# Kernel optimization log

Hardware: AMD Instinct MI355X
Metric: run time of the kernel (lower is better)

The kernel has to match this reference:

```python
import jax, jax.numpy as jnp
import numpy as np

B, N, DIM = 8, 4096, 768
HEADS = 12
HEAD_DIM = DIM // HEADS  # 64
EXP = 2                  # expansion_ratio
EDIM = EXP * DIM         # 1536


def setup_inputs() -> dict:
    key = jax.random.key(0)
    ks = jax.random.split(key, 7)
    s = lambda fan_in: 1.0 / np.sqrt(fan_in)
    return {
        "x": jax.random.normal(ks[0], (B, N, DIM), jnp.float32),
        "w_q": jax.random.normal(ks[1], (DIM, DIM), jnp.float32) * s(DIM),
        "w_kv": jax.random.normal(ks[2], (DIM, 2 * DIM), jnp.float32) * s(DIM),
        "w_proj": jax.random.normal(ks[3], (EDIM, DIM), jnp.float32) * s(EDIM),
        "b_proj": jax.random.normal(ks[4], (DIM,), jnp.float32) * 0.01,
        "w_lepe": jax.random.normal(ks[5], (EDIM, 1, 3, 3), jnp.float32) * s(9),
        "b_lepe": jax.random.normal(ks[6], (EDIM,), jnp.float32) * 0.01,
    }


def _expand_heads(t):
    # t: (B, M, C). roll last axis by -head_dim//2 (the i=1 step of the
    # head-expansion trick with r_int=2), concat -> (B, M, 2C), then split
    # into 2*HEADS heads of HEAD_DIM and move heads to axis 1.
    rolled = jnp.roll(t, -(HEAD_DIM // 2), axis=-1)
    e = jnp.concatenate([t, rolled], axis=-1)  # (B, M, 2C)
    Bb, M, _ = e.shape
    return jnp.swapaxes(e.reshape(Bb, M, EXP * HEADS, HEAD_DIM), 1, 2)  # (B, 2h, M, d)


def reference(x, w_q, w_kv, w_proj, b_proj, w_lepe, b_lepe):
    Bb, Nn, C = x.shape
    ed = EXP * C
    # kv projection -> k, v: (B, h, N, d)
    kv = (x @ w_kv).reshape(Bb, Nn, 2, HEADS, HEAD_DIM)
    k = jnp.swapaxes(kv[:, :, 0], 1, 2)
    v = jnp.swapaxes(kv[:, :, 1], 1, 2)
    # q projection + head expansion -> (B, 2h, N, d)
    q = x @ w_q
    eq = _expand_heads(q)
    # LePE: depthwise 3x3 conv on expanded_q laid out as (B, 2C, H, W)
    H = int(round(Nn ** 0.5))
    qc = jnp.swapaxes(eq, 2, 3).reshape(Bb, ed, H, H)
    lepe = jax.lax.conv_general_dilated(
        qc, w_lepe, window_strides=(1, 1), padding='SAME',
        dimension_numbers=('NCHW', 'OIHW', 'NCHW'), feature_group_count=ed)
    lepe = (lepe + b_lepe[None, :, None, None]).reshape(Bb, ed, Nn)
    lepe = jnp.swapaxes(lepe, 1, 2)  # (B, N, 2C)
    # linear attention: softmax over head_dim, precompute K^T V (d x d)
    ks = jax.nn.softmax(k, axis=3)                      # softmax over feature dim d
    ktv = jnp.einsum('bhnd,bhne->bhde', ks, v)          # (B, h, d, d)
    ektv = _expand_heads(jnp.swapaxes(ktv, 1, 2).reshape(Bb, HEAD_DIM, C))  # (B, 2h, d, d)
    attn = jnp.einsum('bhnd,bhde->bhne', eq, ektv)      # (B, 2h, N, d)
    scale = HEAD_DIM ** -0.5
    out = jnp.swapaxes(scale * attn, 1, 2).reshape(Bb, Nn, ed)  # (B, N, 2C)
    return (out + lepe) @ w_proj + b_proj
```

## Files before the change

kernel.cpp:

```cpp
#include <hip/hip_runtime.h>

#define NB 8
#define NTOK 4096
#define CDIM 768
#define EDIM 1536
#define NHEADS 12
#define HD 64
#define TOTTOK (NB * NTOK)
#define KSPLIT 8

typedef float floatx4 __attribute__((ext_vector_type(4)));
typedef __bf16 bf16x8 __attribute__((ext_vector_type(8)));

__device__ __forceinline__ void gld16(const __bf16* g, void* l) {
  __builtin_amdgcn_global_load_lds(
      (const __attribute__((address_space(1))) unsigned int*)g,
      (__attribute__((address_space(3))) unsigned int*)l, 16, 0, 0);
}

#define MFMA16(a, b, c) __builtin_amdgcn_mfma_f32_16x16x32_bf16(a, b, c, 0, 0, 0)
#define FENCE() asm volatile("" ::: "memory")
#define BARRIER() do { FENCE(); __builtin_amdgcn_s_barrier(); FENCE(); } while (0)

__global__ __launch_bounds__(256) void f32_to_bf16_kernel(
    const float* __restrict__ in, __bf16* __restrict__ out, long n) {
  long i = ((long)blockIdx.x * 256 + threadIdx.x) * 4;
  if (i >= n) return;
  float4 f = *(const float4*)(in + i);
  alignas(8) __bf16 h[4];
  h[0] = (__bf16)f.x; h[1] = (__bf16)f.y; h[2] = (__bf16)f.z; h[3] = (__bf16)f.w;
  *(unsigned long long*)(out + i) = *(const unsigned long long*)h;
}

__global__ __launch_bounds__(256) void transpose_w_kernel(
    const float* __restrict__ W, __bf16* __restrict__ Wt, int K, int N) {
  __shared__ float tile[32][33];
  int nb = blockIdx.x * 32, kb = blockIdx.y * 32;
  int tx = threadIdx.x & 31, ty = threadIdx.x >> 5;
  #pragma unroll
  for (int i = ty; i < 32; i += 8)
    tile[i][tx] = W[(long)(kb + i) * N + nb + tx];
  __syncthreads();
  #pragma unroll
  for (int i = ty; i < 32; i += 8)
    Wt[(long)(nb + i) * K + kb + tx] = (__bf16)tile[tx][i];
}

__global__ __launch_bounds__(512, 2) void gemm256_kernel(
    const __bf16* __restrict__ A, const __bf16* __restrict__ Bt,
    void* __restrict__ C0, void* __restrict__ C1,
    const float* __restrict__ bias,
    int M, int N, int K, int nxb, int mode) {
  __shared__ __bf16 As[2][256 * 64];
  __shared__ __bf16 Bs[2][256 * 64];
  const int tid = threadIdx.x;
  const int wave = tid >> 6, lane = tid & 63;

  const int flat = blockIdx.x;
  const int xcd = flat & 7, rem = flat >> 3;
  const int per = (M >> 8) >> 3;
  const int yb = xcd * per + rem / nxb;
  const int xb = rem % nxb;
  const long m0 = (long)yb * 256;
  const int n0 = xb * 256;

  const int wm = (wave >> 2) * 128;
  const int wn = (wave & 3) * 64;

  const int srow = lane >> 3;
  const int gchunk = (lane & 7) ^ srow;
  const __bf16* Ag = A + (m0 + wave * 8 + srow) * (long)K + gchunk * 8;
  const __bf16* Bg = Bt + ((long)n0 + wave * 8 + srow) * (long)K + gchunk * 8;
  const long slabK = 64 * (long)K;

  const int fr = lane & 15, qh = lane >> 4;
  const int c0 = ((qh ^ (fr & 7)) << 3);
  const int c1 = (((qh + 4) ^ (fr & 7)) << 3);

  floatx4 acc[8][4] = {};
  bf16x8 afl[4][2], bf01[2][2], bf23[2][2];
  const int nt = K >> 6;

  {
    char* al = (char*)&As[0][0] + wave * 1024;
    char* bl = (char*)&Bs[0][0] + wave * 1024;
    gld16(Bg + 0 * slabK, bl + 0 * 8192);
    gld16(Bg + 1 * slabK, bl + 1 * 8192);
    gld16(Bg + 2 * slabK, bl + 2 * 8192);
    gld16(Bg + 3 * slabK, bl + 3 * 8192);
    gld16(Ag + 0 * slabK, al + 0 * 8192);
    gld16(Ag + 2 * slabK, al + 2 * 8192);
    gld16(Ag + 1 * slabK, al + 1 * 8192);
    gld16(Ag + 3 * slabK, al + 3 * 8192);
  }
  asm volatile("s_waitcnt vmcnt(2)" ::: "memory");
  BARRIER();

  for (int t = 0; t < nt; ++t) {
    const int cur = t & 1;
    const bool pf = (t + 1 < nt);
    const __bf16* Ac = &As[cur][0];
    const __bf16* Bc = &Bs[cur][0];
    const __bf16* an = Ag + (t + 1) * 64;
    const __bf16* bn = Bg + (t + 1) * 64;
    char* al = (char*)&As[cur ^ 1][0] + wave * 1024;
    char* bl = (char*)&Bs[cur ^ 1][0] + wave * 1024;

    #pragma unroll
    for (int i = 0; i < 4; ++i) {
      const __bf16* p = &Ac[(wm + i * 16 + fr) * 64];
      afl[i][0] = *(const bf16x8*)(p + c0);
      afl[i][1] = *(const bf16x8*)(p + c1);
    }
    #pragma unroll
    for (int j = 0; j < 2; ++j) {
      const __bf16* p = &Bc[(wn + j * 16 + fr) * 64];
      bf01[j][0] = *(const bf16x8*)(p + c0);
      bf01[j][1] = *(const bf16x8*)(p + c1);
    }
    if (pf) { gld16(bn + 0 * slabK, bl + 0 * 8192);
              gld16(bn + 1 * slabK, bl + 1 * 8192); }
    BARRIER();
    asm volatile("s_waitcnt lgkmcnt(0)");
    __builtin_amdgcn_sched_barrier(0);
    __builtin_amdgcn_s_setprio(1);
    #pragma unroll
    for (int i = 0; i < 4; ++i)
      #pragma unroll
      for (int j = 0; j < 2; ++j) {
        acc[i][j] = MFMA16(afl[i][0], bf01[j][0], acc[i][j]);
        acc[i][j] = MFMA16(afl[i][1], bf01[j][1], acc[i][j]);
      }
    __builtin_amdgcn_s_setprio(0);
    BARRIER();

    #pragma unroll
    for (int j = 0; j < 2; ++j) {
      const __bf16* p = &Bc[(wn + (2 + j) * 16 + fr) * 64];
      bf23[j][0] = *(const bf16x8*)(p + c0);
      bf23[j][1] = *(const bf16x8*)(p + c1);
    }
    if (pf) {
      gld16(bn + 2 * slabK, bl + 2 * 8192);
      gld16(bn + 3 * slabK, bl + 3 * 8192);
      asm volatile("s_waitcnt vmcnt(4)" ::: "memory");
    } else {
      asm volatile("s_waitcnt vmcnt(0)" ::: "memory");
    }
    BARRIER();
    asm volatile("s_waitcnt lgkmcnt(0)");
    __builtin_amdgcn_sched_barrier(0);
    __builtin_amdgcn_s_setprio(1);
    #pragma unroll
    for (int i = 0; i < 4; ++i)
      #pragma unroll
      for (int j = 0; j < 2; ++j) {
        acc[i][2 + j] = MFMA16(afl[i][0], bf23[j][0], acc[i][2 + j]);
        acc[i][2 + j] = MFMA16(afl[i][1], bf23[j][1], acc[i][2 + j]);
      }
    __builtin_amdgcn_s_setprio(0);
    BARRIER();

    #pragma unroll
    for (int i = 0; i < 4; ++i) {
      const __bf16* p = &Ac[(wm + (4 + i) * 16 + fr) * 64];
      afl[i][0] = *(const bf16x8*)(p + c0);
      afl[i][1] = *(const bf16x8*)(p + c1);
    }
    if (pf) { gld16(an + 0 * slabK, al + 0 * 8192);
              gld16(an + 2 * slabK, al + 2 * 8192); }
    BARRIER();
    asm volatile("s_waitcnt lgkmcnt(0)");
    __builtin_amdgcn_sched_barrier(0);
    __builtin_amdgcn_s_setprio(1);
    #pragma unroll
    for (int i = 0; i < 4; ++i)
      #pragma unroll
      for (int j = 0; j < 2; ++j) {
        acc[4 + i][2 + j] = MFMA16(afl[i][0], bf23[j][0], acc[4 + i][2 + j]);
        acc[4 + i][2 + j] = MFMA16(afl[i][1], bf23[j][1], acc[4 + i][2 + j]);
      }
    __builtin_amdgcn_s_setprio(0);
    BARRIER();

    if (pf) {
      gld16(an + 1 * slabK, al + 1 * 8192);
      gld16(an + 3 * slabK, al + 3 * 8192);
      asm volatile("s_waitcnt vmcnt(2)" ::: "memory");
    }
    BARRIER();
    asm volatile("s_waitcnt lgkmcnt(0)");
    __builtin_amdgcn_sched_barrier(0);
    __builtin_amdgcn_s_setprio(1);
    #pragma unroll
    for (int i = 0; i < 4; ++i)
      #pragma unroll
      for (int j = 0; j < 2; ++j) {
        acc[4 + i][j] = MFMA16(afl[i][0], bf01[j][0], acc[4 + i][j]);
        acc[4 + i][j] = MFMA16(afl[i][1], bf01[j][1], acc[4 + i][j]);
      }
    __builtin_amdgcn_s_setprio(0);
    BARRIER();
  }

  const int col = lane & 15, rq = (lane >> 4) * 4;
  if (mode == 1) {
    #pragma unroll
    for (int j = 0; j < 4; ++j) {
      const int gn = n0 + wn + j * 16 + col;
      const float bj = bias[gn];
      #pragma unroll
      for (int i = 0; i < 8; ++i)
        #pragma unroll
        for (int r = 0; r < 4; ++r)
          ((float*)C0)[(m0 + wm + i * 16 + rq + r) * (long)N + gn] =
              acc[i][j][r] + bj;
    }
  } else {
    const bool qhalf = (n0 + 256 <= CDIM);
    __bf16* Cb = qhalf ? (__bf16*)C0 : (__bf16*)C1;
    const long cstride = qhalf ? CDIM : EDIM;
    const int ncol0 = qhalf ? (n0 + wn) : (n0 + wn - CDIM);
    __bf16* S = &As[0][0] + wave * (16 * 76);
    const int er = lane >> 2, ec = (lane & 3) * 8;
    #pragma unroll
    for (int i = 0; i < 8; ++i) {
      #pragma unroll
      for (int j = 0; j < 4; ++j)
        #pragma unroll
        for (int r = 0; r < 4; ++r)
          S[(rq + r) * 76 + j * 16 + col] = (__bf16)acc[i][j][r];
      asm volatile("s_waitcnt lgkmcnt(0)" ::: "memory");
      __builtin_amdgcn_sched_barrier(0);
      uint4 v0 = *(const uint4*)&S[er * 76 + ec];
      uint4 v1 = *(const uint4*)&S[er * 76 + ec + 32];
      __bf16* dst = Cb + (m0 + wm + i * 16 + er) * cstride + ncol0;
      *(uint4*)(dst + ec) = v0;
      *(uint4*)(dst + ec + 32) = v1;
      asm volatile("s_waitcnt lgkmcnt(0)" ::: "memory");
      __builtin_amdgcn_sched_barrier(0);
    }
  }
}

__global__ __launch_bounds__(256) void gemm_glds_kernel(
    const __bf16* __restrict__ A, const __bf16* __restrict__ Bt,
    void* __restrict__ C0, void* __restrict__ C1,
    const float* __restrict__ bias,
    int M, int N, int K, int nxb, int mode) {
  __shared__ __bf16 As[128 * 32];
  __shared__ __bf16 Bs[128 * 32];
  const int tid = threadIdx.x;
  const int wave = tid >> 6, lane = tid & 63;

  const int flat = blockIdx.x;
  const int xcd = flat & 7, rem = flat >> 3;
  const int per = (M >> 7) >> 3;
  const int yb = xcd * per + rem / nxb;
  const int xb = rem % nxb;
  const long m0 = (long)yb * 128;
  const int n0 = xb * 128;

  const int wm = (wave >> 1) * 64, wn = (wave & 1) * 64;

  const int srow = lane >> 2;
  const int gchunk = (lane & 3) ^ ((lane >> 3) & 3);
  const __bf16* Ag = A + (m0 + wave * 16 + srow) * (long)K + gchunk * 8;
  const __bf16* Bg = Bt + ((long)n0 + wave * 16 + srow) * (long)K + gchunk * 8;
  char* Al = (char*)As + wave * 16 * 64;
  char* Bl = (char*)Bs + wave * 16 * 64;
  const long rowskip = 64 * (long)K;

  const int fr = lane & 15;
  const int csw = ((lane >> 4) ^ ((fr >> 1) & 3)) * 8;

  floatx4 acc[4][4] = {};

  for (int k0 = 0; k0 < K; k0 += 32) {
    __syncthreads();
    gld16(Ag + k0, Al);
    gld16(Ag + k0 + rowskip, Al + 64 * 64);
    gld16(Bg + k0, Bl);
    gld16(Bg + k0 + rowskip, Bl + 64 * 64);
    __syncthreads();
    bf16x8 af[4], bfr[4];
    #pragma unroll
    for (int i = 0; i < 4; ++i)
      af[i] = *(const bf16x8*)&As[(wm + i * 16 + fr) * 32 + csw];
    #pragma unroll
    for (int j = 0; j < 4; ++j)
      bfr[j] = *(const bf16x8*)&Bs[(wn + j * 16 + fr) * 32 + csw];
    #pragma unroll
    for (int i = 0; i < 4; ++i)
      #pragma unroll
      for (int j = 0; j < 4; ++j)
        acc[i][j] = __builtin_amdgcn_mfma_f32_16x16x32_bf16(af[i], bfr[j], acc[i][j], 0, 0, 0);
  }

  const int col = lane & 15, rq = (lane >> 4) * 4;
  if (mode == 1) {
    #pragma unroll
    for (int i = 0; i < 4; ++i)
      #pragma unroll
      for (int j = 0; j < 4; ++j)
        #pragma unroll
        for (int r = 0; r < 4; ++r) {
          long gm = m0 + wm + i * 16 + rq + r;
          int gn = n0 + wn + j * 16 + col;
          ((float*)C0)[gm * N + gn] = acc[i][j][r] + bias[gn];
        }
  } else {
    if (n0 + 128 <= CDIM) {
      #pragma unroll
      for (int i = 0; i < 4; ++i)
        #pragma unroll
        for (int j = 0; j < 4; ++j)
          #pragma unroll
          for (int r = 0; r < 4; ++r) {
            long gm = m0 + wm + i * 16 + rq + r;
            int gn = n0 + wn + j * 16 + col;
            ((__bf16*)C0)[gm * CDIM + gn] = (__bf16)acc[i][j][r];
          }
    } else {
      #pragma unroll
      for (int i = 0; i < 4; ++i)
        #pragma unroll
        for (int j = 0; j < 4; ++j)
          #pragma unroll
          for (int r = 0; r < 4; ++r) {
            long gm = m0 + wm + i * 16 + rq + r;
            int gn = n0 + wn + j * 16 + col - CDIM;
            ((__bf16*)C1)[gm * EDIM + gn] = (__bf16)acc[i][j][r];
          }
    }
  }
}

__global__ __launch_bounds__(256) void ktv_kernel(
    const __bf16* __restrict__ kv, float* __restrict__ ktv_part) {
  const int split = blockIdx.x, h = blockIdx.y, b = blockIdx.z;
  __shared__ __bf16 As[64 * 40];
  __shared__ __bf16 Bs[64 * 40];
  const int tid = threadIdx.x, wave = tid >> 6, lane = tid & 63;
  const int sn = tid >> 3;
  const int sc = (tid & 7) * 8;
  const int fr = lane & 15, fk = (lane >> 4) * 8;
  floatx4 acc[4] = {};
  const long rowbase = (long)b * NTOK * EDIM;
  const int span = NTOK / KSPLIT;

  for (int n0 = split * span; n0 < split * span + span; n0 += 32) {
    __syncthreads();
    const __bf16* krow = kv + rowbase + (long)(n0 + sn) * EDIM + h * HD + sc;
    const __bf16* vrow = krow + CDIM;
    uint4 ku = *(const uint4*)krow;
    uint4 vu = *(const uint4*)vrow;
    const __bf16* kh = (const __bf16*)&ku;
    const __bf16* vh = (const __bf16*)&vu;
    float kf[8];
    float mx = -1e30f;
    #pragma unroll
    for (int j = 0; j < 8; ++j) { kf[j] = (float)kh[j]; mx = fmaxf(mx, kf[j]); }
    #pragma unroll
    for (int m = 1; m < 8; m <<= 1) mx = fmaxf(mx, __shfl_xor(mx, m));
    float s = 0.f;
    #pragma unroll
    for (int j = 0; j < 8; ++j) { kf[j] = __expf(kf[j] - mx); s += kf[j]; }
    #pragma unroll
    for (int m = 1; m < 8; m <<= 1) s += __shfl_xor(s, m);
    const float inv = 1.f / s;
    #pragma unroll
    for (int j = 0; j < 8; ++j) {
      As[(sc + j) * 40 + sn] = (__bf16)(kf[j] * inv);
      Bs[(sc + j) * 40 + sn] = vh[j];
    }
    __syncthreads();
    bf16x8 af = *(const bf16x8*)&As[(wave * 16 + fr) * 40 + fk];
    #pragma unroll
    for (int j = 0; j < 4; ++j) {
      bf16x8 bf_ = *(const bf16x8*)&Bs[(j * 16 + fr) * 40 + fk];
      acc[j] = __builtin_amdgcn_mfma_f32_16x16x32_bf16(af, bf_, acc[j], 0, 0, 0);
    }
  }

  const int col = lane & 15, rq = (lane >> 4) * 4;
  long base = (((long)split * NB + b) * NHEADS + h) * (HD * HD);
  #pragma unroll
  for (int j = 0; j < 4; ++j)
    #pragma unroll
    for (int r = 0; r < 4; ++r)
      ktv_part[base + (wave * 16 + rq + r) * HD + j * 16 + col] = acc[j][r];
}

__global__ __launch_bounds__(256) void ektv_kernel(
    const float* __restrict__ ktv_part, __bf16* __restrict__ ektv) {
  int idx = blockIdx.x * 256 + threadIdx.x;
  int e = idx & 63;
  int d = (idx >> 6) & 63;
  int H = (idx >> 12) % 24;
  int b = idx / 98304;
  int c = H * 64 + e;
  int cp = (c < CDIM) ? c : (c - CDIM + 32) % CDIM;
  int hs = cp >> 6, es = cp & 63;
  long o = (((long)b * NHEADS + hs) * HD + d) * HD + es;
  float s = 0.f;
  #pragma unroll
  for (int sp = 0; sp < KSPLIT; ++sp)
    s += ktv_part[(long)sp * (NB * NHEADS * HD * HD) + o];
  long ob = ((long)(idx >> 12)) * (HD * HD) + (long)e * HD + d;
  ektv[ob] = (__bf16)s;
}

__global__ __launch_bounds__(256) void attn_kernel(
    const __bf16* __restrict__ q, const __bf16* __restrict__ ektv,
    __bf16* __restrict__ mid) {
  const int tt = blockIdx.x, H = blockIdx.y, b = blockIdx.z;
  __shared__ __bf16 As[128 * 72];
  __shared__ __bf16 Bs[64 * 72];
  const int tid = threadIdx.x, wave = tid >> 6, lane = tid & 63;
  const int qbase = (H < NHEADS) ? H * 64 : (H - NHEADS) * 64 + 32;
  const long n0 = (long)b * NTOK + tt * 128;

  {
    int nl = tid >> 1, d0 = (tid & 1) * 32;
    const __bf16* qrow = q + (n0 + nl) * CDIM;
    #pragma unroll
    for (int cch = 0; cch < 4; ++cch) {
      int d = d0 + cch * 8;
      int c0 = qbase + d;
      if (c0 >= CDIM) c0 -= CDIM;
      *(uint4*)&As[nl * 72 + d] = *(const uint4*)(qrow + c0);
    }
  }
  {
    int e = tid >> 2, ch4 = (tid & 3) * 8;
    const __bf16* src = ektv + ((long)b * 24 + H) * (HD * HD) + e * HD;
    *(uint4*)&Bs[e * 72 + ch4] = *(const uint4*)(src + ch4);
    *(uint4*)&Bs[e * 72 + ch4 + 32] = *(const uint4*)(src + ch4 + 32);
  }
  __syncthreads();

  floatx4 acc[2][4] = {};
  const int fr = lane & 15, fk = (lane >> 4) * 8;
  const int wm = wave * 32;
  #pragma unroll
  for (int kk = 0; kk < 64; kk += 32) {
    bf16x8 af0 = *(const bf16x8*)&As[(wm + fr) * 72 + kk + fk];
    bf16x8 af1 = *(const bf16x8*)&As[(wm + 16 + fr) * 72 + kk + fk];
    #pragma unroll
    for (int j = 0; j < 4; ++j) {
      bf16x8 bf_ = *(const bf16x8*)&Bs[(j * 16 + fr) * 72 + kk + fk];
      acc[0][j] = __builtin_amdgcn_mfma_f32_16x16x32_bf16(af0, bf_, acc[0][j], 0, 0, 0);
      acc[1][j] = __builtin_amdgcn_mfma_f32_16x16x32_bf16(af1, bf_, acc[1][j], 0, 0, 0);
    }
  }

  const int col = lane & 15, rq = (lane >> 4) * 4;
  const float scale = 0.125f;
  #pragma unroll
  for (int i = 0; i < 2; ++i)
    #pragma unroll
    for (int j = 0; j < 4; ++j)
      #pragma unroll
      for (int r = 0; r < 4; ++r) {
        long n = n0 + wm + i * 16 + rq + r;
        mid[n * EDIM + H * 64 + j * 16 + col] = (__bf16)(acc[i][j][r] * scale);
      }
}

__global__ __launch_bounds__(256) void lepe_kernel(
    const __bf16* __restrict__ q, const float* __restrict__ w_lepe,
    const float* __restrict__ b_lepe, __bf16* __restrict__ mid) {
  __shared__ __bf16 smem[6 * 64 * 64];
  const int g = blockIdx.x, yg = blockIdx.y, b = blockIdx.z;
  const int y0 = yg * 4;
  const int tid = threadIdx.x;

  #pragma unroll
  for (int k = 0; k < 12; ++k) {
    int v = tid + k * 256;
    int r = v >> 9;
    int rem = v & 511;
    int x = rem >> 3;
    int chv = (rem & 7) * 8;
    int yy = y0 + r - 1;
    uint4 val = {0u, 0u, 0u, 0u};
    if (yy >= 0 && yy < 64)
      val = *(const uint4*)(q + ((long)(b * NTOK + yy * 64 + x)) * CDIM + g * 64 + chv);
    *(uint4*)&smem[r * 4096 + x * 64 + chv] = val;
  }
  __syncthreads();

  const int ch = tid & 63, xg = tid >> 6;
  const int cq = g * 64 + ch;
  const int c2 = CDIM + ((cq + 736) % CDIM);
  float w1[9], w2[9];
  #pragma unroll
  for (int j = 0; j < 9; ++j) {
    w1[j] = w_lepe[cq * 9 + j];
    w2[j] = w_lepe[c2 * 9 + j];
  }
  const float bias1 = b_lepe[cq], bias2 = b_lepe[c2];

  const int x0 = xg * 16;
  float cm[6], cc[6], cp[6];
  #pragma unroll
  for (int r = 0; r < 6; ++r) {
    cm[r] = (x0 > 0) ? (float)smem[r * 4096 + (x0 - 1) * 64 + ch] : 0.f;
    cc[r] = (float)smem[r * 4096 + x0 * 64 + ch];
  }
  #pragma unroll
  for (int i = 0; i < 16; ++i) {
    const int x = x0 + i;
    #pragma unroll
    for (int r = 0; r < 6; ++r)
      cp[r] = (x < 63) ? (float)smem[r * 4096 + (x + 1) * 64 + ch] : 0.f;
    #pragma unroll
    for (int ly = 0; ly < 4; ++ly) {
      float a1 = bias1, a2 = bias2;
      #pragma unroll
      for (int r = 0; r < 3; ++r) {
        const float vm = cm[ly + r], vc = cc[ly + r], vp = cp[ly + r];
        a1 += w1[r * 3 + 0] * vm + w1[r * 3 + 1] * vc + w1[r * 3 + 2] * vp;
        a2 += w2[r * 3 + 0] * vm + w2[r * 3 + 1] * vc + w2[r * 3 + 2] * vp;
      }
      long o = ((long)(b * NTOK + (y0 + ly) * 64 + x)) * EDIM;
      mid[o + cq] = (__bf16)((float)mid[o + cq] + a1);
      mid[o + c2] = (__bf16)((float)mid[o + c2] + a2);
    }
    #pragma unroll
    for (int r = 0; r < 6; ++r) { cm[r] = cc[r]; cc[r] = cp[r]; }
  }
}

extern "C" void kernel_launch(void* const* d_in, const int* in_sizes, int n_in,
                              void* d_out, int out_size, void* d_ws, size_t ws_size,
                              hipStream_t stream) {
  const float* x      = (const float*)d_in[0];
  const float* w_q    = (const float*)d_in[1];
  const float* w_kv   = (const float*)d_in[2];
  const float* w_proj = (const float*)d_in[3];
  const float* b_proj = (const float*)d_in[4];
  const float* w_lepe = (const float*)d_in[5];
  const float* b_lepe = (const float*)d_in[6];
  float* out = (float*)d_out;

  char* ws = (char*)d_ws;
  __bf16* Wt_qkv = (__bf16*)ws; ws += (long)(CDIM + EDIM) * CDIM * 2;
  __bf16* Wt_p   = (__bf16*)ws; ws += (long)CDIM * EDIM * 2;
  __bf16* xb     = (__bf16*)ws; ws += (long)TOTTOK * CDIM * 2;
  __bf16* qb     = (__bf16*)ws; ws += (long)TOTTOK * CDIM * 2;
  __bf16* kvb    = (__bf16*)ws; ws += (long)TOTTOK * EDIM * 2;
  float*  ktv_part = (float*)ws; ws += (long)KSPLIT * NB * NHEADS * HD * HD * 4;
  __bf16* ektv   = (__bf16*)ws; ws += (long)NB * 24 * HD * HD * 2;
  __bf16* mid = kvb;

  f32_to_bf16_kernel<<<(TOTTOK * CDIM) / (256 * 4), 256, 0, stream>>>(
      x, xb, (long)TOTTOK * CDIM);
  transpose_w_kernel<<<dim3(CDIM / 32, CDIM / 32), 256, 0, stream>>>(
      w_q, Wt_qkv, CDIM, CDIM);
  transpose_w_kernel<<<dim3(EDIM / 32, CDIM / 32), 256, 0, stream>>>(
      w_kv, Wt_qkv + (long)CDIM * CDIM, CDIM, EDIM);
  transpose_w_kernel<<<dim3(CDIM / 32, EDIM / 32), 256, 0, stream>>>(
      w_proj, Wt_p, EDIM, CDIM);
  gemm256_kernel<<<(TOTTOK / 256) * 9, 512, 0, stream>>>(
      xb, Wt_qkv, qb, kvb, nullptr, TOTTOK, CDIM + EDIM, CDIM, 9, 0);
  ktv_kernel<<<dim3(KSPLIT, NHEADS, NB), 256, 0, stream>>>(kvb, ktv_part);
  ektv_kernel<<<(NB * 24 * HD * HD) / 256, 256, 0, stream>>>(ktv_part, ektv);
  attn_kernel<<<dim3(NTOK / 128, 24, NB), 256, 0, stream>>>(qb, ektv, mid);
  lepe_kernel<<<dim3(12, 16, NB), 256, 0, stream>>>(qb, w_lepe, b_lepe, mid);
  gemm_glds_kernel<<<(TOTTOK / 128) * 6, 256, 0, stream>>>(
      mid, Wt_p, out, nullptr, b_proj, TOTTOK, CDIM, EDIM, 6, 1);
}
```

Baseline: 595.9 us.

## Fuse LePE depthwise conv into attention kernel epilogue

```diff
diff --git a/kernel.cpp b/kernel.cpp
--- a/kernel.cpp
+++ b/kernel.cpp
@@ -411,25 +411,36 @@
   ektv[ob] = (__bf16)s;
 }
 
-__global__ __launch_bounds__(256) void attn_kernel(
+__global__ __launch_bounds__(256) void attn_lepe_kernel(
     const __bf16* __restrict__ q, const __bf16* __restrict__ ektv,
+    const float* __restrict__ w_lepe, const float* __restrict__ b_lepe,
     __bf16* __restrict__ mid) {
   const int tt = blockIdx.x, H = blockIdx.y, b = blockIdx.z;
-  __shared__ __bf16 As[128 * 72];
+  __shared__ __bf16 Qs[256 * 72];
   __shared__ __bf16 Bs[64 * 72];
   const int tid = threadIdx.x, wave = tid >> 6, lane = tid & 63;
   const int qbase = (H < NHEADS) ? H * 64 : (H - NHEADS) * 64 + 32;
+  const int y0 = tt * 2;
   const long n0 = (long)b * NTOK + tt * 128;
 
   {
     int nl = tid >> 1, d0 = (tid & 1) * 32;
-    const __bf16* qrow = q + (n0 + nl) * CDIM;
-    #pragma unroll
-    for (int cch = 0; cch < 4; ++cch) {
-      int d = d0 + cch * 8;
-      int c0 = qbase + d;
-      if (c0 >= CDIM) c0 -= CDIM;
-      *(uint4*)&As[nl * 72 + d] = *(const uint4*)(qrow + c0);
+    #pragma unroll
+    for (int rep = 0; rep < 2; ++rep) {
+      int tok = rep * 128 + nl;
+      int iy = y0 - 1 + (tok >> 6);
+      bool valid = (iy >= 0 && iy < 64);
+      int iyc = valid ? iy : 0;
+      const __bf16* qrow = q + ((long)b * NTOK + iyc * 64 + (tok & 63)) * CDIM;
+      #pragma unroll
+      for (int cch = 0; cch < 4; ++cch) {
+        int d = d0 + cch * 8;
+        int c0 = qbase + d;
+        if (c0 >= CDIM) c0 -= CDIM;
+        uint4 v = {0u, 0u, 0u, 0u};
+        if (valid) v = *(const uint4*)(qrow + c0);
+        *(uint4*)&Qs[tok * 72 + d] = v;
+      }
     }
   }
   {
@@ -445,8 +456,8 @@
   const int wm = wave * 32;
   #pragma unroll
   for (int kk = 0; kk < 64; kk += 32) {
-    bf16x8 af0 = *(const bf16x8*)&As[(wm + fr) * 72 + kk + fk];
-    bf16x8 af1 = *(const bf16x8*)&As[(wm + 16 + fr) * 72 + kk + fk];
+    bf16x8 af0 = *(const bf16x8*)&Qs[(64 + wm + fr) * 72 + kk + fk];
+    bf16x8 af1 = *(const bf16x8*)&Qs[(64 + wm + 16 + fr) * 72 + kk + fk];
     #pragma unroll
     for (int j = 0; j < 4; ++j) {
       bf16x8 bf_ = *(const bf16x8*)&Bs[(j * 16 + fr) * 72 + kk + fk];
@@ -455,81 +466,47 @@
     }
   }
 
-  const int col = lane & 15, rq = (lane >> 4) * 4;
+  const int col = lane & 15, rq4 = (lane >> 4) * 4;
   const float scale = 0.125f;
-  #pragma unroll
-  for (int i = 0; i < 2; ++i)
-    #pragma unroll
-    for (int j = 0; j < 4; ++j)
+  float wf[4][9], bf[4];
+  #pragma unroll
+  for (int j = 0; j < 4; ++j) {
+    int c = H * 64 + j * 16 + col;
+    #pragma unroll
+    for (int t = 0; t < 9; ++t) wf[j][t] = w_lepe[c * 9 + t];
+    bf[j] = b_lepe[c];
+  }
+
+  #pragma unroll
+  for (int i = 0; i < 2; ++i) {
+    const int ln0 = wm + i * 16 + rq4;
+    const int ly = ln0 >> 6, lx0 = ln0 & 63;
+    #pragma unroll
+    for (int j = 0; j < 4; ++j) {
+      const int d = j * 16 + col;
+      float win[3][6];
+      #pragma unroll
+      for (int dr = 0; dr < 3; ++dr) {
+        const int rowb = (ly + dr) * 64;
+        #pragma unroll
+        for (int s = 0; s < 6; ++s) {
+          int xx = lx0 - 1 + s;
+          win[dr][s] = (xx >= 0 && xx < 64)
+                           ? (float)Qs[(rowb + xx) * 72 + d] : 0.f;
+        }
+      }
       #pragma unroll
       for (int r = 0; r < 4; ++r) {
-        long n = n0 + wm + i * 16 + rq + r;
-        mid[n * EDIM + H * 64 + j * 16 + col] = (__bf16)(acc[i][j][r] * scale);
-      }
-}
-
-__global__ __launch_bounds__(256) void lepe_kernel(
-    const __bf16* __restrict__ q, const float* __restrict__ w_lepe,
-    const float* __restrict__ b_lepe, __bf16* __restrict__ mid) {
-  __shared__ __bf16 smem[6 * 64 * 64];
-  const int g = blockIdx.x, yg = blockIdx.y, b = blockIdx.z;
-  const int y0 = yg * 4;
-  const int tid = threadIdx.x;
-
-  #pragma unroll
-  for (int k = 0; k < 12; ++k) {
-    int v = tid + k * 256;
-    int r = v >> 9;
-    int rem = v & 511;
-    int x = rem >> 3;
-    int chv = (rem & 7) * 8;
-    int yy = y0 + r - 1;
-    uint4 val = {0u, 0u, 0u, 0u};
-    if (yy >= 0 && yy < 64)
-      val = *(const uint4*)(q + ((long)(b * NTOK + yy * 64 + x)) * CDIM + g * 64 + chv);
-    *(uint4*)&smem[r * 4096 + x * 64 + chv] = val;
-  }
-  __syncthreads();
-
-  const int ch = tid & 63, xg = tid >> 6;
-  const int cq = g * 64 + ch;
-  const int c2 = CDIM + ((cq + 736) % CDIM);
-  float w1[9], w2[9];
-  #pragma unroll
-  for (int j = 0; j < 9; ++j) {
-    w1[j] = w_lepe[cq * 9 + j];
-    w2[j] = w_lepe[c2 * 9 + j];
-  }
-  const float bias1 = b_lepe[cq], bias2 = b_lepe[c2];
-
-  const int x0 = xg * 16;
-  float cm[6], cc[6], cp[6];
-  #pragma unroll
-  for (int r = 0; r < 6; ++r) {
-    cm[r] = (x0 > 0) ? (float)smem[r * 4096 + (x0 - 1) * 64 + ch] : 0.f;
-    cc[r] = (float)smem[r * 4096 + x0 * 64 + ch];
-  }
-  #pragma unroll
-  for (int i = 0; i < 16; ++i) {
-    const int x = x0 + i;
-    #pragma unroll
-    for (int r = 0; r < 6; ++r)
-      cp[r] = (x < 63) ? (float)smem[r * 4096 + (x + 1) * 64 + ch] : 0.f;
-    #pragma unroll
-    for (int ly = 0; ly < 4; ++ly) {
-      float a1 = bias1, a2 = bias2;
-      #pragma unroll
-      for (int r = 0; r < 3; ++r) {
-        const float vm = cm[ly + r], vc = cc[ly + r], vp = cp[ly + r];
-        a1 += w1[r * 3 + 0] * vm + w1[r * 3 + 1] * vc + w1[r * 3 + 2] * vp;
-        a2 += w2[r * 3 + 0] * vm + w2[r * 3 + 1] * vc + w2[r * 3 + 2] * vp;
-      }
-      long o = ((long)(b * NTOK + (y0 + ly) * 64 + x)) * EDIM;
-      mid[o + cq] = (__bf16)((float)mid[o + cq] + a1);
-      mid[o + c2] = (__bf16)((float)mid[o + c2] + a2);
-    }
-    #pragma unroll
-    for (int r = 0; r < 6; ++r) { cm[r] = cc[r]; cc[r] = cp[r]; }
+        float conv = bf[j];
+        #pragma unroll
+        for (int dr = 0; dr < 3; ++dr)
+          conv += wf[j][dr * 3 + 0] * win[dr][r] +
+                  wf[j][dr * 3 + 1] * win[dr][r + 1] +
+                  wf[j][dr * 3 + 2] * win[dr][r + 2];
+        long n = n0 + ln0 + r;
+        mid[n * EDIM + H * 64 + d] = (__bf16)(acc[i][j][r] * scale + conv);
+      }
+    }
   }
 }
 
@@ -567,8 +544,8 @@
       xb, Wt_qkv, qb, kvb, nullptr, TOTTOK, CDIM + EDIM, CDIM, 9, 0);
   ktv_kernel<<<dim3(KSPLIT, NHEADS, NB), 256, 0, stream>>>(kvb, ktv_part);
   ektv_kernel<<<(NB * 24 * HD * HD) / 256, 256, 0, stream>>>(ktv_part, ektv);
-  attn_kernel<<<dim3(NTOK / 128, 24, NB), 256, 0, stream>>>(qb, ektv, mid);
-  lepe_kernel<<<dim3(12, 16, NB), 256, 0, stream>>>(qb, w_lepe, b_lepe, mid);
+  attn_lepe_kernel<<<dim3(NTOK / 128, 24, NB), 256, 0, stream>>>(
+      qb, ektv, w_lepe, b_lepe, mid);
   gemm_glds_kernel<<<(TOTTOK / 128) * 6, 256, 0, stream>>>(
       mid, Wt_p, out, nullptr, b_proj, TOTTOK, CDIM, EDIM, 6, 1);
 }
```

Result: faster. 531.6 us (-10.8%).
